# Optimization experiments

Hardware: AMD Instinct MI355X
Metric: run time of the kernel (lower is better)

The kernel has to match this reference:

```python
import jax, jax.numpy as jnp
import numpy as np
import math

NH = 16  # n_head
HS = 64  # head_size = n_embd // n_head


def setup_inputs() -> dict:
    key = jax.random.key(0)
    ks = jax.random.split(key, 7)
    B, T, C, QL, KVL = 2, 2048, 1024, 128, 128
    s = lambda k, shape, fan_in: jax.random.normal(k, shape, jnp.float32) / np.sqrt(fan_in)
    return {
        "x": jax.random.normal(ks[0], (B, T, C), jnp.float32),
        "W_dq": s(ks[1], (QL, C), C),
        "W_uq": s(ks[2], (C, QL), QL),
        "W_dkv": s(ks[3], (KVL, C), C),
        "W_uk": s(ks[4], (C, KVL), KVL),
        "W_uv": s(ks[5], (C, KVL), KVL),
        "W_o": s(ks[6], (C, C), C),
    }


def reference(x, W_dq, W_uq, W_dkv, W_uk, W_uv, W_o):
    B, T, C = x.shape
    kvl = W_dkv.shape[0]
    # absorbed matrices (training branch)
    k_eff = (W_dq.T @ W_uq.T @ W_uk).reshape(NH, HS, kvl)            # (nh, hs, kvl)
    v_eff = (W_uv.T @ W_o.T).reshape(kvl, NH, HS).transpose(1, 0, 2)  # (nh, kvl, hs)
    # latent kv cache
    c_kv = x @ W_dkv.T                                                # (B, T, kvl)
    # query path
    q = (x @ W_dq.T @ W_uq.T).reshape(B, T, NH, HS).transpose(0, 2, 1, 3)  # (B, nh, T, hs)
    # scores: q @ k_eff @ c_kv^T
    ql = jnp.einsum('bhtd,hdl->bhtl', q, k_eff)                       # (B, nh, T, kvl)
    scores = jnp.einsum('bhtl,bsl->bhts', ql, c_kv) / math.sqrt(HS)   # (B, nh, T, T)
    # causal mask
    mask = jnp.tril(jnp.ones((T, T), dtype=bool))
    scores = jnp.where(mask[None, None], scores, -jnp.inf)
    attn = jax.nn.softmax(scores, axis=-1)
    # output: attn @ c_kv @ v_eff
    ctx = jnp.einsum('bhts,bsl->bhtl', attn, c_kv)                    # (B, nh, T, kvl)
    y = jnp.einsum('bhtl,hld->bhtd', ctx, v_eff)                      # (B, nh, T, hs)
    y = y.transpose(0, 2, 1, 3).reshape(B, T, C)
    return y, c_kv
```

## Files before the change

kernel.cpp:

```cpp
#include <hip/hip_runtime.h>
#include <hip/hip_bf16.h>

typedef __hip_bfloat16 bf16;
typedef __attribute__((ext_vector_type(8))) short short8;
typedef __attribute__((ext_vector_type(4))) float f32x4;

#define NHD 16
#define HSD 64
#define KVLD 128
#define QLD 128
#define CD 1024
#define BD 2
#define TD 2048

__device__ __forceinline__ short8 ld8(const bf16* p) { return *(const short8*)p; }
__device__ __forceinline__ void st8(bf16* p, short8 v) { *(short8*)p = v; }

__device__ __forceinline__ short8 cvt8(float4 a, float4 b) {
    union { short8 s; bf16 h[8]; } u;
    u.h[0] = __float2bfloat16(a.x); u.h[1] = __float2bfloat16(a.y);
    u.h[2] = __float2bfloat16(a.z); u.h[3] = __float2bfloat16(a.w);
    u.h[4] = __float2bfloat16(b.x); u.h[5] = __float2bfloat16(b.y);
    u.h[6] = __float2bfloat16(b.z); u.h[7] = __float2bfloat16(b.w);
    return u.s;
}
__device__ __forceinline__ void st4(bf16* p, float4 a) {
    union { short4 s; bf16 h[4]; } u;
    u.h[0] = __float2bfloat16(a.x); u.h[1] = __float2bfloat16(a.y);
    u.h[2] = __float2bfloat16(a.z); u.h[3] = __float2bfloat16(a.w);
    *(short4*)p = u.s;
}
__device__ __forceinline__ void st4f(bf16* p, f32x4 a) {
    union { short4 s; bf16 h[4]; } u;
    u.h[0] = __float2bfloat16(a[0]); u.h[1] = __float2bfloat16(a[1]);
    u.h[2] = __float2bfloat16(a[2]); u.h[3] = __float2bfloat16(a[3]);
    *(short4*)p = u.s;
}


__global__ __launch_bounds__(256) void k_m1p(const float* __restrict__ wuq,
                                             const float* __restrict__ wuk,
                                             float* __restrict__ m1p) {
    int idx = blockIdx.x * 256 + threadIdx.x;
    int i = idx >> 7, j = idx & 127;
    int c0 = blockIdx.y * 128;
    float acc = 0.f;
    for (int c = c0; c < c0 + 128; ++c)
        acc += wuq[c * QLD + i] * wuk[c * KVLD + j];
    m1p[blockIdx.y * 16384 + idx] = acc;
}

__global__ __launch_bounds__(256) void k_m1r(const float* __restrict__ m1p,
                                             float* __restrict__ m1) {
    int idx = blockIdx.x * 256 + threadIdx.x;
    float acc = 0.f;
#pragma unroll
    for (int p = 0; p < 8; ++p) acc += m1p[p * 16384 + idx];
    m1[idx] = acc;
}

__global__ __launch_bounds__(256) void k_keff(const float* __restrict__ wdq,
                                              const float* __restrict__ m1,
                                              float* __restrict__ keff) {
    int idx = blockIdx.x * 256 + threadIdx.x;
    int c = idx >> 7, j = idx & 127;
    float acc = 0.f;
    for (int i = 0; i < QLD; ++i)
        acc += wdq[i * CD + c] * m1[i * KVLD + j];
    keff[idx] = acc;
}

__global__ __launch_bounds__(256) void k_veff(const float* __restrict__ wuv,
                                              const float* __restrict__ wo,
                                              bf16* __restrict__ veffT_bf) {
    int idx = blockIdx.x * 256 + threadIdx.x;
    int l = idx & 127;
    int cc = idx >> 7;
    float acc = 0.f;
    for (int c0 = 0; c0 < CD; ++c0)
        acc += wuv[c0 * KVLD + l] * wo[(size_t)cc * CD + c0];
    veffT_bf[idx] = __float2bfloat16(acc);
}

__global__ __launch_bounds__(256) void k_E(const float* __restrict__ wuq,
                                           const float* __restrict__ keff,
                                           bf16* __restrict__ Et_bf) {
    int idx = blockIdx.x * 256 + threadIdx.x;
    int i = idx & 127;
    int l = (idx >> 7) & 127;
    int h = idx >> 14;
    float acc = 0.f;
    for (int d = 0; d < HSD; ++d)
        acc += wuq[(h * HSD + d) * QLD + i] * keff[(h * HSD + d) * KVLD + l];
    Et_bf[idx] = __float2bfloat16(0.1803368801f * acc);
}

__global__ __launch_bounds__(256) void k_proj(const float* __restrict__ x,
                                              const float* __restrict__ wdq,
                                              const float* __restrict__ wdkv,
                                              bf16* __restrict__ q1_bf,
                                              float* __restrict__ ckv_out,
                                              bf16* __restrict__ ckv_bf,
                                              bf16* __restrict__ ckvT_bf) {
    const int m0 = blockIdx.x * 16;
    const int tid = threadIdx.x;
    const int w = tid >> 6, lane = tid & 63, m16 = lane & 15, g = lane >> 4;

    __shared__ __align__(16) short As_raw[16 * 72];
    __shared__ __align__(16) short Bs_raw[256 * 72];
    bf16* As = (bf16*)As_raw;
    bf16* Bs = (bf16*)Bs_raw;

    f32x4 acc[4];
#pragma unroll
    for (int nb = 0; nb < 4; ++nb) acc[nb] = (f32x4){0.f, 0.f, 0.f, 0.f};

    for (int k0 = 0; k0 < CD; k0 += 64) {
        __syncthreads();
        {
            int row = tid >> 4, kc = (tid & 15) << 2;
            float4 f = *(const float4*)(x + (size_t)(m0 + row) * CD + k0 + kc);
            st4(As + row * 72 + kc, f);
        }
#pragma unroll
        for (int kk = 0; kk < 8; ++kk) {
            int v = tid + kk * 256;
            int row = v >> 3, kc = (v & 7) << 3;
            const float* wr = (row < 128) ? (wdq + (size_t)row * CD)
                                          : (wdkv + (size_t)(row - 128) * CD);
            const float* src = wr + k0 + kc;
            float4 f0 = *(const float4*)(src);
            float4 f1 = *(const float4*)(src + 4);
            st8(Bs + row * 72 + kc, cvt8(f0, f1));
        }
        __syncthreads();
        short8 aF[2];
#pragma unroll
        for (int kf = 0; kf < 2; ++kf)
            aF[kf] = ld8(As + m16 * 72 + kf * 32 + g * 8);
#pragma unroll
        for (int nb = 0; nb < 4; ++nb)
#pragma unroll
            for (int kf = 0; kf < 2; ++kf) {
                short8 bF = ld8(Bs + (w * 64 + nb * 16 + m16) * 72 + kf * 32 + g * 8);
                acc[nb] = __builtin_amdgcn_mfma_f32_16x16x32_bf16(aF[kf], bF, acc[nb], 0, 0, 0);
            }
    }

#pragma unroll
    for (int nb = 0; nb < 4; ++nb)
#pragma unroll
        for (int r = 0; r < 4; ++r) {
            int t = m0 + g * 4 + r;
            int col = w * 64 + nb * 16 + m16;
            float v = acc[nb][r];
            if (col < 128) {
                q1_bf[(size_t)t * QLD + col] = __float2bfloat16(v);
            } else {
                int l = col - 128;
                ckv_out[(size_t)t * KVLD + l] = v;
                bf16 hv = __float2bfloat16(v);
                ckv_bf[(size_t)t * KVLD + l] = hv;
                int b = t >> 11, tl = t & 2047;
                ckvT_bf[((size_t)b * KVLD + l) * TD + tl] = hv;
            }
        }
}

__global__ __launch_bounds__(256, 3) void k_flash(const bf16* __restrict__ Q1_bf,
                                                  const bf16* __restrict__ Et_bf,
                                                  const bf16* __restrict__ ckv_bf,
                                                  const bf16* __restrict__ ckvT_bf,
                                                  const bf16* __restrict__ veffT_bf,
                                                  float* __restrict__ yout) {
    const int h = blockIdx.x & 15;
    const int b = blockIdx.x >> 4;
    const int qt = 31 - blockIdx.y;
    const int tid = threadIdx.x;
    const int w = tid >> 6;
    const int lane = tid & 63;
    const int m16 = lane & 15;
    const int g = lane >> 4;
    const int row0 = qt * 64;

    __shared__ __align__(16) short smem_raw[23680];
    bf16* smem = (bf16*)smem_raw;
    bf16* kvN = smem;
    bf16* kvT = smem + 8704;
    bf16* pS  = smem + 19072 + w * 1152;
    bf16* qlS = smem + 8704;
    bf16* ctxS = smem;
    bf16* vT   = smem + 8704;

    {
        const bf16 one = __float2bfloat16(1.0f);
        for (int i = tid; i < 16 * 72; i += 256)
            kvT[9216 + i] = one;
    }

    {
        const bf16* q1src = Q1_bf + ((size_t)(b * TD + row0)) * QLD;
#pragma unroll
        for (int k = 0; k < 4; ++k) {
            int v = tid + k * 256;
            int row = v >> 4, cv = (v & 15) << 3;
            st8(kvN + row * 136 + cv, ld8(q1src + row * QLD + cv));
        }
    }
    __syncthreads();
    {
        short8 aq[4];
#pragma unroll
        for (int kf = 0; kf < 4; ++kf)
            aq[kf] = ld8(kvN + (w * 16 + m16) * 136 + kf * 32 + g * 8);
        const bf16* Eh = Et_bf + (size_t)h * QLD * KVLD;
        f32x4 qc[8];
#pragma unroll
        for (int nb = 0; nb < 8; ++nb) qc[nb] = (f32x4){0.f, 0.f, 0.f, 0.f};
#pragma unroll
        for (int nb = 0; nb < 8; ++nb)
#pragma unroll
            for (int kf = 0; kf < 4; ++kf) {
                short8 bq = ld8(Eh + (nb * 16 + m16) * QLD + kf * 32 + g * 8);
                qc[nb] = __builtin_amdgcn_mfma_f32_16x16x32_bf16(aq[kf], bq, qc[nb], 0, 0, 0);
            }
#pragma unroll
        for (int nb = 0; nb < 8; ++nb)
#pragma unroll
            for (int r = 0; r < 4; ++r)
                qlS[(w * 16 + g * 4 + r) * 136 + nb * 16 + m16] = __float2bfloat16(qc[nb][r]);
    }
    __syncthreads();
    short8 qlA[4];
#pragma unroll
    for (int kf = 0; kf < 4; ++kf)
        qlA[kf] = ld8(qlS + (w * 16 + m16) * 136 + kf * 32 + g * 8);

    f32x4 cx[9];
#pragma unroll
    for (int nb = 0; nb < 9; ++nb) cx[nb] = (f32x4){0.f, 0.f, 0.f, 0.f};
    float mrow = -INFINITY;
    const int rg = row0 + w * 16 + m16;

    const bf16* ckb = ckv_bf + (size_t)b * TD * KVLD;
    const bf16* ckTb = ckvT_bf + (size_t)b * KVLD * TD;

    int nrow[4], ncol[4], trow[4], tcol[4];
#pragma unroll
    for (int k = 0; k < 4; ++k) {
        int v = tid + k * 256;
        nrow[k] = v >> 4; ncol[k] = (v & 15) << 3;
        trow[k] = v >> 3; tcol[k] = (v & 7) << 3;
    }
    short8 pfN[4], pfT[4];
#pragma unroll
    for (int k = 0; k < 4; ++k) {
        pfN[k] = ld8(ckb + (size_t)nrow[k] * KVLD + ncol[k]);
        pfT[k] = ld8(ckTb + (size_t)trow[k] * TD + tcol[k]);
    }

    for (int tile = 0; tile <= qt; ++tile) {
        const int s0 = tile * 64;
        const bool diag = (tile == qt);
        __syncthreads();
#pragma unroll
        for (int k = 0; k < 4; ++k) {
            st8(kvN + nrow[k] * 136 + ncol[k], pfN[k]);
            st8(kvT + trow[k] * 72 + tcol[k], pfT[k]);
        }
        __syncthreads();
        if (tile < qt) {
            const int s1 = s0 + 64;
#pragma unroll
            for (int k = 0; k < 4; ++k) {
                pfN[k] = ld8(ckb + (size_t)(s1 + nrow[k]) * KVLD + ncol[k]);
                pfT[k] = ld8(ckTb + (size_t)trow[k] * TD + s1 + tcol[k]);
            }
        }

        f32x4 sa[4];
#pragma unroll
        for (int nb = 0; nb < 4; ++nb) sa[nb] = (f32x4){0.f, 0.f, 0.f, 0.f};
#pragma unroll
        for (int nb = 0; nb < 4; ++nb)
#pragma unroll
            for (int kf = 0; kf < 4; ++kf) {
                short8 ak = ld8(kvN + (nb * 16 + m16) * 136 + kf * 32 + g * 8);
                sa[nb] = __builtin_amdgcn_mfma_f32_16x16x32_bf16(ak, qlA[kf], sa[nb], 0, 0, 0);
            }

        if (diag) {
#pragma unroll
            for (int nb = 0; nb < 4; ++nb)
#pragma unroll
                for (int r = 0; r < 4; ++r) {
                    int sg = s0 + nb * 16 + g * 4 + r;
                    if (sg > rg) sa[nb][r] = -INFINITY;
                }
        }

        float mloc = sa[0][0];
#pragma unroll
        for (int nb = 0; nb < 4; ++nb)
#pragma unroll
            for (int r = 0; r < 4; ++r) mloc = fmaxf(mloc, sa[nb][r]);
        mloc = fmaxf(mloc, __shfl_xor(mloc, 16));
        mloc = fmaxf(mloc, __shfl_xor(mloc, 32));
        if (__any(mloc > mrow)) {
            float mt = fmaxf(mrow, mloc);
            float al = exp2f(mrow - mt);
            mrow = mt;
#pragma unroll
            for (int nb = 0; nb < 9; ++nb)
#pragma unroll
                for (int r = 0; r < 4; ++r) cx[nb][r] *= al;
        }

#pragma unroll
        for (int nb = 0; nb < 4; ++nb) {
            float4 p4;
            p4.x = exp2f(sa[nb][0] - mrow);
            p4.y = exp2f(sa[nb][1] - mrow);
            p4.z = exp2f(sa[nb][2] - mrow);
            p4.w = exp2f(sa[nb][3] - mrow);
            st4(pS + m16 * 72 + nb * 16 + g * 4, p4);
        }
        __builtin_amdgcn_wave_barrier();

        short8 pA[2];
#pragma unroll
        for (int kf = 0; kf < 2; ++kf)
            pA[kf] = ld8(pS + m16 * 72 + kf * 32 + g * 8);
#pragma unroll
        for (int nb = 0; nb < 9; ++nb)
#pragma unroll
            for (int kf = 0; kf < 2; ++kf) {
                short8 av = ld8(kvT + (nb * 16 + m16) * 72 + kf * 32 + g * 8);
                cx[nb] = __builtin_amdgcn_mfma_f32_16x16x32_bf16(av, pA[kf], cx[nb], 0, 0, 0);
            }
    }

    float invl = 1.f / cx[8][0];
#pragma unroll
    for (int nb = 0; nb < 8; ++nb)
#pragma unroll
        for (int r = 0; r < 4; ++r) cx[nb][r] *= invl;
    __syncthreads();
#pragma unroll
    for (int nb = 0; nb < 8; ++nb)
        st4f(ctxS + (w * 16 + m16) * 136 + nb * 16 + g * 4, cx[nb]);
    {
        const bf16* vsrc = veffT_bf + (size_t)h * HSD * KVLD;
#pragma unroll
        for (int k = 0; k < 4; ++k) {
            int v = tid + k * 256;
            int row = v >> 4, cv = (v & 15) << 3;
            st8(vT + row * 136 + cv, ld8(vsrc + row * KVLD + cv));
        }
    }
    __syncthreads();

    short8 cB[4];
#pragma unroll
    for (int kf = 0; kf < 4; ++kf)
        cB[kf] = ld8(ctxS + (w * 16 + m16) * 136 + kf * 32 + g * 8);
    f32x4 ya[4];
#pragma unroll
    for (int nb = 0; nb < 4; ++nb) ya[nb] = (f32x4){0.f, 0.f, 0.f, 0.f};
#pragma unroll
    for (int nb = 0; nb < 4; ++nb)
#pragma unroll
        for (int kf = 0; kf < 4; ++kf) {
            short8 av = ld8(vT + (nb * 16 + m16) * 136 + kf * 32 + g * 8);
            ya[nb] = __builtin_amdgcn_mfma_f32_16x16x32_bf16(av, cB[kf], ya[nb], 0, 0, 0);
        }
    float* yo = yout + ((size_t)b * TD + rg) * CD + h * HSD;
#pragma unroll
    for (int nb = 0; nb < 4; ++nb)
        *(float4*)(yo + nb * 16 + g * 4) = *(float4*)&ya[nb];
}

extern "C" void kernel_launch(void* const* d_in, const int* in_sizes, int n_in,
                              void* d_out, int out_size, void* d_ws, size_t ws_size,
                              hipStream_t stream) {
    const float* x    = (const float*)d_in[0];
    const float* wdq  = (const float*)d_in[1];
    const float* wuq  = (const float*)d_in[2];
    const float* wdkv = (const float*)d_in[3];
    const float* wuk  = (const float*)d_in[4];
    const float* wuv  = (const float*)d_in[5];
    const float* wo   = (const float*)d_in[6];
    float* yout = (float*)d_out;
    float* ckv_out = yout + (size_t)BD * TD * CD;

    float* ws = (float*)d_ws;
    float* M1   = ws;
    float* M1P  = M1 + 16384;
    float* keff = M1P + 131072;
    bf16* Et_bf    = (bf16*)(keff + 131072);
    bf16* veffT_bf = Et_bf + 262144;
    bf16* ckv_bf   = veffT_bf + 131072;
    bf16* ckvT_bf  = ckv_bf + 524288;
    bf16* Q1_bf    = ckvT_bf + 524288;

    dim3 m1grid(64, 8);
    k_m1p <<<m1grid, 256, 0, stream>>>(wuq, wuk, M1P);
    k_m1r <<<64,   256, 0, stream>>>(M1P, M1);
    k_keff<<<512,  256, 0, stream>>>(wdq, M1, keff);
    k_veff<<<512,  256, 0, stream>>>(wuv, wo, veffT_bf);
    k_E   <<<1024, 256, 0, stream>>>(wuq, keff, Et_bf);

    k_proj<<<TD * BD / 16, 256, 0, stream>>>(x, wdq, wdkv, Q1_bf, ckv_out, ckv_bf, ckvT_bf);

    dim3 grid(32, 32);
    k_flash<<<grid, 256, 0, stream>>>(Q1_bf, Et_bf, ckv_bf, ckvT_bf, veffT_bf, yout);
}
```

Baseline: 266.9 us.

## Pair low and high causal query tiles in one 512-thread flash block

Each flash block now runs 8 waves that handle two query tiles, a late tile (qhi) and an early tile (qlo). They share the K/V tiles streamed into LDS, and the qlo waves skip compute once past their causal limit. The aim is to balance causal work across blocks, halve the grid and reuse each loaded KV tile for two query tiles. The cost is that the qlo waves sit idle at barriers for the remaining tiles, and the 512-thread launch bound with a larger LDS footprint may cut occupancy or force register spills.

```diff
diff --git a/kernel.cpp b/kernel.cpp
--- a/kernel.cpp
+++ b/kernel.cpp
@@ -167,7 +167,7 @@
         }
 }
 
-__global__ __launch_bounds__(256, 3) void k_flash(const bf16* __restrict__ Q1_bf,
+__global__ __launch_bounds__(512, 4) void k_flash(const bf16* __restrict__ Q1_bf,
                                                   const bf16* __restrict__ Et_bf,
                                                   const bf16* __restrict__ ckv_bf,
                                                   const bf16* __restrict__ ckvT_bf,
@@ -175,44 +175,50 @@
                                                   float* __restrict__ yout) {
     const int h = blockIdx.x & 15;
     const int b = blockIdx.x >> 4;
-    const int qt = 31 - blockIdx.y;
+    const int qlo = blockIdx.y;
+    const int qhi = 31 - qlo;
     const int tid = threadIdx.x;
     const int w = tid >> 6;
+    const int ws = w >> 2;
+    const int wq = w & 3;
     const int lane = tid & 63;
     const int m16 = lane & 15;
     const int g = lane >> 4;
-    const int row0 = qt * 64;
-
-    __shared__ __align__(16) short smem_raw[23680];
+    const int myqt = ws ? qlo : qhi;
+    const int row0 = myqt * 64;
+
+    __shared__ __align__(16) short smem_raw[28288];
     bf16* smem = (bf16*)smem_raw;
     bf16* kvN = smem;
     bf16* kvT = smem + 8704;
     bf16* pS  = smem + 19072 + w * 1152;
-    bf16* qlS = smem + 8704;
-    bf16* ctxS = smem;
-    bf16* vT   = smem + 8704;
+    bf16* bufLo = kvT;
+    bf16* vT = smem + 19072;
 
     {
         const bf16 one = __float2bfloat16(1.0f);
-        for (int i = tid; i < 16 * 72; i += 256)
-            kvT[9216 + i] = one;
+        for (int idx = tid; idx < 16 * 72; idx += 512)
+            kvT[9216 + idx] = one;
     }
 
     {
-        const bf16* q1src = Q1_bf + ((size_t)(b * TD + row0)) * QLD;
-#pragma unroll
-        for (int k = 0; k < 4; ++k) {
-            int v = tid + k * 256;
+        const bf16* q1hi = Q1_bf + ((size_t)(b * TD + qhi * 64)) * QLD;
+        const bf16* q1lo = Q1_bf + ((size_t)(b * TD + qlo * 64)) * QLD;
+#pragma unroll
+        for (int k = 0; k < 2; ++k) {
+            int v = tid + k * 512;
             int row = v >> 4, cv = (v & 15) << 3;
-            st8(kvN + row * 136 + cv, ld8(q1src + row * QLD + cv));
+            st8(kvN + row * 136 + cv, ld8(q1hi + row * QLD + cv));
+            st8(bufLo + row * 136 + cv, ld8(q1lo + row * QLD + cv));
         }
     }
     __syncthreads();
+    bf16* myQ1 = ws ? bufLo : kvN;
     {
         short8 aq[4];
 #pragma unroll
         for (int kf = 0; kf < 4; ++kf)
-            aq[kf] = ld8(kvN + (w * 16 + m16) * 136 + kf * 32 + g * 8);
+            aq[kf] = ld8(myQ1 + (wq * 16 + m16) * 136 + kf * 32 + g * 8);
         const bf16* Eh = Et_bf + (size_t)h * QLD * KVLD;
         f32x4 qc[8];
 #pragma unroll
@@ -224,120 +230,122 @@
                 short8 bq = ld8(Eh + (nb * 16 + m16) * QLD + kf * 32 + g * 8);
                 qc[nb] = __builtin_amdgcn_mfma_f32_16x16x32_bf16(aq[kf], bq, qc[nb], 0, 0, 0);
             }
+        __syncthreads();
 #pragma unroll
         for (int nb = 0; nb < 8; ++nb)
 #pragma unroll
             for (int r = 0; r < 4; ++r)
-                qlS[(w * 16 + g * 4 + r) * 136 + nb * 16 + m16] = __float2bfloat16(qc[nb][r]);
+                myQ1[(wq * 16 + g * 4 + r) * 136 + nb * 16 + m16] = __float2bfloat16(qc[nb][r]);
     }
     __syncthreads();
     short8 qlA[4];
 #pragma unroll
     for (int kf = 0; kf < 4; ++kf)
-        qlA[kf] = ld8(qlS + (w * 16 + m16) * 136 + kf * 32 + g * 8);
+        qlA[kf] = ld8(myQ1 + (wq * 16 + m16) * 136 + kf * 32 + g * 8);
 
     f32x4 cx[9];
 #pragma unroll
     for (int nb = 0; nb < 9; ++nb) cx[nb] = (f32x4){0.f, 0.f, 0.f, 0.f};
     float mrow = -INFINITY;
-    const int rg = row0 + w * 16 + m16;
+    const int rg = row0 + wq * 16 + m16;
 
     const bf16* ckb = ckv_bf + (size_t)b * TD * KVLD;
     const bf16* ckTb = ckvT_bf + (size_t)b * KVLD * TD;
 
-    int nrow[4], ncol[4], trow[4], tcol[4];
-#pragma unroll
-    for (int k = 0; k < 4; ++k) {
-        int v = tid + k * 256;
+    int nrow[2], ncol[2], trow[2], tcol[2];
+#pragma unroll
+    for (int k = 0; k < 2; ++k) {
+        int v = tid + k * 512;
         nrow[k] = v >> 4; ncol[k] = (v & 15) << 3;
         trow[k] = v >> 3; tcol[k] = (v & 7) << 3;
     }
-    short8 pfN[4], pfT[4];
-#pragma unroll
-    for (int k = 0; k < 4; ++k) {
+    short8 pfN[2], pfT[2];
+#pragma unroll
+    for (int k = 0; k < 2; ++k) {
         pfN[k] = ld8(ckb + (size_t)nrow[k] * KVLD + ncol[k]);
         pfT[k] = ld8(ckTb + (size_t)trow[k] * TD + tcol[k]);
     }
 
-    for (int tile = 0; tile <= qt; ++tile) {
+    for (int tile = 0; tile <= qhi; ++tile) {
         const int s0 = tile * 64;
-        const bool diag = (tile == qt);
         __syncthreads();
 #pragma unroll
-        for (int k = 0; k < 4; ++k) {
+        for (int k = 0; k < 2; ++k) {
             st8(kvN + nrow[k] * 136 + ncol[k], pfN[k]);
             st8(kvT + trow[k] * 72 + tcol[k], pfT[k]);
         }
         __syncthreads();
-        if (tile < qt) {
+        if (tile < qhi) {
             const int s1 = s0 + 64;
 #pragma unroll
-            for (int k = 0; k < 4; ++k) {
+            for (int k = 0; k < 2; ++k) {
                 pfN[k] = ld8(ckb + (size_t)(s1 + nrow[k]) * KVLD + ncol[k]);
                 pfT[k] = ld8(ckTb + (size_t)trow[k] * TD + s1 + tcol[k]);
             }
         }
 
-        f32x4 sa[4];
-#pragma unroll
-        for (int nb = 0; nb < 4; ++nb) sa[nb] = (f32x4){0.f, 0.f, 0.f, 0.f};
-#pragma unroll
-        for (int nb = 0; nb < 4; ++nb)
-#pragma unroll
-            for (int kf = 0; kf < 4; ++kf) {
-                short8 ak = ld8(kvN + (nb * 16 + m16) * 136 + kf * 32 + g * 8);
-                sa[nb] = __builtin_amdgcn_mfma_f32_16x16x32_bf16(ak, qlA[kf], sa[nb], 0, 0, 0);
-            }
-
-        if (diag) {
+        if (ws == 0 || tile <= qlo) {
+            f32x4 sa[4];
+#pragma unroll
+            for (int nb = 0; nb < 4; ++nb) sa[nb] = (f32x4){0.f, 0.f, 0.f, 0.f};
 #pragma unroll
             for (int nb = 0; nb < 4; ++nb)
 #pragma unroll
-                for (int r = 0; r < 4; ++r) {
-                    int sg = s0 + nb * 16 + g * 4 + r;
-                    if (sg > rg) sa[nb][r] = -INFINITY;
+                for (int kf = 0; kf < 4; ++kf) {
+                    short8 ak = ld8(kvN + (nb * 16 + m16) * 136 + kf * 32 + g * 8);
+                    sa[nb] = __builtin_amdgcn_mfma_f32_16x16x32_bf16(ak, qlA[kf], sa[nb], 0, 0, 0);
                 }
-        }
-
-        float mloc = sa[0][0];
-#pragma unroll
-        for (int nb = 0; nb < 4; ++nb)
-#pragma unroll
-            for (int r = 0; r < 4; ++r) mloc = fmaxf(mloc, sa[nb][r]);
-        mloc = fmaxf(mloc, __shfl_xor(mloc, 16));
-        mloc = fmaxf(mloc, __shfl_xor(mloc, 32));
-        if (__any(mloc > mrow)) {
-            float mt = fmaxf(mrow, mloc);
-            float al = exp2f(mrow - mt);
-            mrow = mt;
+
+            if (tile == myqt) {
+#pragma unroll
+                for (int nb = 0; nb < 4; ++nb)
+#pragma unroll
+                    for (int r = 0; r < 4; ++r) {
+                        int sg = s0 + nb * 16 + g * 4 + r;
+                        if (sg > rg) sa[nb][r] = -INFINITY;
+                    }
+            }
+
+            float mloc = sa[0][0];
+#pragma unroll
+            for (int nb = 0; nb < 4; ++nb)
+#pragma unroll
+                for (int r = 0; r < 4; ++r) mloc = fmaxf(mloc, sa[nb][r]);
+            mloc = fmaxf(mloc, __shfl_xor(mloc, 16));
+            mloc = fmaxf(mloc, __shfl_xor(mloc, 32));
+            if (__any(mloc > mrow)) {
+                float mt = fmaxf(mrow, mloc);
+                float al = exp2f(mrow - mt);
+                mrow = mt;
+#pragma unroll
+                for (int nb = 0; nb < 9; ++nb)
+#pragma unroll
+                    for (int r = 0; r < 4; ++r) cx[nb][r] *= al;
+            }
+
+#pragma unroll
+            for (int nb = 0; nb < 4; ++nb) {
+                float4 p4;
+                p4.x = exp2f(sa[nb][0] - mrow);
+                p4.y = exp2f(sa[nb][1] - mrow);
+                p4.z = exp2f(sa[nb][2] - mrow);
+                p4.w = exp2f(sa[nb][3] - mrow);
+                st4(pS + m16 * 72 + nb * 16 + g * 4, p4);
+            }
+            __builtin_amdgcn_wave_barrier();
+
+            short8 pA[2];
+#pragma unroll
+            for (int kf = 0; kf < 2; ++kf)
+                pA[kf] = ld8(pS + m16 * 72 + kf * 32 + g * 8);
 #pragma unroll
             for (int nb = 0; nb < 9; ++nb)
 #pragma unroll
-                for (int r = 0; r < 4; ++r) cx[nb][r] *= al;
-        }
-
-#pragma unroll
-        for (int nb = 0; nb < 4; ++nb) {
-            float4 p4;
-            p4.x = exp2f(sa[nb][0] - mrow);
-            p4.y = exp2f(sa[nb][1] - mrow);
-            p4.z = exp2f(sa[nb][2] - mrow);
-            p4.w = exp2f(sa[nb][3] - mrow);
-            st4(pS + m16 * 72 + nb * 16 + g * 4, p4);
-        }
-        __builtin_amdgcn_wave_barrier();
-
-        short8 pA[2];
-#pragma unroll
-        for (int kf = 0; kf < 2; ++kf)
-            pA[kf] = ld8(pS + m16 * 72 + kf * 32 + g * 8);
-#pragma unroll
-        for (int nb = 0; nb < 9; ++nb)
-#pragma unroll
-            for (int kf = 0; kf < 2; ++kf) {
-                short8 av = ld8(kvT + (nb * 16 + m16) * 72 + kf * 32 + g * 8);
-                cx[nb] = __builtin_amdgcn_mfma_f32_16x16x32_bf16(av, pA[kf], cx[nb], 0, 0, 0);
-            }
+                for (int kf = 0; kf < 2; ++kf) {
+                    short8 av = ld8(kvT + (nb * 16 + m16) * 72 + kf * 32 + g * 8);
+                    cx[nb] = __builtin_amdgcn_mfma_f32_16x16x32_bf16(av, pA[kf], cx[nb], 0, 0, 0);
+                }
+        }
     }
 
     float invl = 1.f / cx[8][0];
@@ -346,14 +354,15 @@
 #pragma unroll
         for (int r = 0; r < 4; ++r) cx[nb][r] *= invl;
     __syncthreads();
+    bf16* ctxS = ws ? bufLo : kvN;
 #pragma unroll
     for (int nb = 0; nb < 8; ++nb)
-        st4f(ctxS + (w * 16 + m16) * 136 + nb * 16 + g * 4, cx[nb]);
+        st4f(ctxS + (wq * 16 + m16) * 136 + nb * 16 + g * 4, cx[nb]);
     {
         const bf16* vsrc = veffT_bf + (size_t)h * HSD * KVLD;
 #pragma unroll
-        for (int k = 0; k < 4; ++k) {
-            int v = tid + k * 256;
+        for (int k = 0; k < 2; ++k) {
+            int v = tid + k * 512;
             int row = v >> 4, cv = (v & 15) << 3;
             st8(vT + row * 136 + cv, ld8(vsrc + row * KVLD + cv));
         }
@@ -363,7 +372,7 @@
     short8 cB[4];
 #pragma unroll
     for (int kf = 0; kf < 4; ++kf)
-        cB[kf] = ld8(ctxS + (w * 16 + m16) * 136 + kf * 32 + g * 8);
+        cB[kf] = ld8(ctxS + (wq * 16 + m16) * 136 + kf * 32 + g * 8);
     f32x4 ya[4];
 #pragma unroll
     for (int nb = 0; nb < 4; ++nb) ya[nb] = (f32x4){0.f, 0.f, 0.f, 0.f};
@@ -412,6 +421,6 @@
 
     k_proj<<<TD * BD / 16, 256, 0, stream>>>(x, wdq, wdkv, Q1_bf, ckv_out, ckv_bf, ckvT_bf);
 
-    dim3 grid(32, 32);
-    k_flash<<<grid, 256, 0, stream>>>(Q1_bf, Et_bf, ckv_bf, ckvT_bf, veffT_bf, yout);
-}
+    dim3 grid(32, 16);
+    k_flash<<<grid, 512, 0, stream>>>(Q1_bf, Et_bf, ckv_bf, ckvT_bf, veffT_bf, yout);
+}
```

New measurement: 263.3 us. Within noise of the previous version (-1.4%).
